# Optimization experiments

Hardware: AMD Instinct MI355X
Metric: run time of the kernel (lower is better)

Reference implementation:

```python
import jax, jax.numpy as jnp
import numpy as np

N = 200000          # nodes
G = 8192            # graphs (data.num_graphs)
NUM_RADIAL = 32
M_OUT = 85          # embedding_depth // 3 -> 85x1o


def setup_inputs() -> dict:
    key = jax.random.key(0)
    ks = jax.random.split(key, 24)
    f32 = jnp.float32
    def rn(k, shape, scale=1.0):
        return jax.random.normal(k, shape, dtype=f32) * scale
    inp = {}
    inp['pos'] = rn(ks[0], (N, 3))
    inp['z'] = jax.random.randint(ks[1], (N,), 0, 100)
    inp['batch'] = jnp.sort(jax.random.randint(ks[2], (N,), 0, G))
    inp['node_table'] = rn(ks[3], (100, 32))
    # MLP weights (fan-in scaled), biases zero
    inp['W_rbf0'] = rn(ks[4], (32, 64), 32 ** -0.5)
    inp['b_rbf0'] = jnp.zeros((64,), f32)
    inp['W_rbf1'] = rn(ks[5], (64, 64), 64 ** -0.5)
    inp['b_rbf1'] = jnp.zeros((64,), f32)
    inp['W_m0'] = rn(ks[6], (96, 64), 96 ** -0.5)
    inp['b_m0'] = jnp.zeros((64,), f32)
    inp['W_m1'] = rn(ks[7], (64, 64), 64 ** -0.5)
    inp['b_m1'] = jnp.zeros((64,), f32)
    inp['W_m2'] = rn(ks[8], (64, 64), 64 ** -0.5)
    inp['b_m2'] = jnp.zeros((64,), f32)
    # e3nn-style weights: N(0,1), path normalization applied in the math
    inp['w_tp0'] = rn(ks[9], (64, 64))   # 0e x 0e -> 0e
    inp['w_tp1'] = rn(ks[10], (64, 64))  # 0e x 1o -> 1o
    inp['w_tp2'] = rn(ks[11], (64, 32))  # 0e x 2e -> 2e
    inp['L0'] = rn(ks[12], (64, 64))     # o3.Linear 0e block
    inp['L1o'] = rn(ks[13], (64, 64))    # o3.Linear 1o block
    inp['L2e'] = rn(ks[14], (32, 32))    # o3.Linear 2e block
    inp['L_out'] = rn(ks[15], (64, 85))  # tl2: 64x1o -> 85x1o
    return inp


def _sph_harm(pos):
    # e3nn real spherical harmonics, normalize=False, normalization='component'
    x, y, z = pos[:, 0], pos[:, 1], pos[:, 2]
    sh0 = jnp.ones_like(x)                              # [N]     l=0
    sh1 = jnp.sqrt(3.0) * pos                           # [N,3]   l=1
    s15 = jnp.sqrt(15.0)
    s5 = jnp.sqrt(5.0)
    sh2 = jnp.stack([
        s15 * x * z,
        s15 * x * y,
        s5 * (y * y - 0.5 * (x * x + z * z)),
        s15 * y * z,
        0.5 * s15 * (z * z - x * x),
    ], axis=-1)                                          # [N,5]   l=2
    return sh0, sh1, sh2


def _forward(pos, z, batch, node_table, W_rbf0, b_rbf0, W_rbf1, b_rbf1,
             W_m0, b_m0, W_m1, b_m1, W_m2, b_m2,
             w_tp0, w_tp1, w_tp2, L0, L1o, L2e, L_out):
    sh0, sh1, sh2 = _sph_harm(pos)  # centroid is zeros

    # Gaussian RBF on |pos|, start=0 stop=1
    dist = jnp.linalg.norm(pos, axis=1)                  # [N]
    offsets = jnp.linspace(0.0, 1.0, NUM_RADIAL)
    coeff = -0.5 / (offsets[1] - offsets[0]) ** 2
    rbf = jnp.exp(coeff * (dist[:, None] - offsets) ** 2)  # [N,32]

    # rbf_emb MLP (1 hidden layer)
    r = jax.nn.gelu(rbf @ W_rbf0 + b_rbf0)
    r = r @ W_rbf1 + b_rbf1                               # [N,64]

    # radial_message MLP (2 hidden layers) on [r_emb, node_emb]
    h = jnp.concatenate([r, node_table[z]], axis=-1)      # [N,96]
    h = jax.nn.gelu(h @ W_m0 + b_m0)
    h = jax.nn.gelu(h @ W_m1 + b_m1)
    msg = h @ W_m2 + b_m2                                 # [N,64]  64x0e

    # FullyConnectedTensorProduct(64x0e, 1x0e+1x1o+1x2e -> irreps_mid)
    # scalar (x) l  -> l ; path norm 1/sqrt(fan_in), fan_in = 64*1
    inv = 1.0 / jnp.sqrt(64.0)
    c0 = (msg @ w_tp0) * sh0[:, None] * inv               # [N,64]    0e
    c1 = (msg @ w_tp1)[:, :, None] * sh1[:, None, :] * inv  # [N,64,3] 1o
    c2 = (msg @ w_tp2)[:, :, None] * sh2[:, None, :] * inv  # [N,32,5] 2e
    # 64x1e and 32x2o output blocks have no allowed paths -> identically zero

    # act1: gelu on scalar (0e) irreps only
    c0 = jax.nn.gelu(c0)

    # scatter mean + scatter sum over graphs
    cnt = jnp.maximum(jax.ops.segment_sum(jnp.ones_like(dist), batch, num_segments=G), 1.0)
    def agg(v, cshape):
        s = jax.ops.segment_sum(v, batch, num_segments=G)
        return s / cnt.reshape(cshape) + s
    g0 = agg(c0, (G, 1))        # [G,64]
    g1 = agg(c1, (G, 1, 1))     # [G,64,3]
    g2 = agg(c2, (G, 1, 1))     # [G,32,5]

    # tl1 (o3.Linear, per-irrep multiplicity mixing, 1/sqrt(mult_in) norm)
    g0 = g0 @ L0 * (64 ** -0.5)
    g1 = jnp.einsum('gum,uv->gvm', g1, L1o) * (64 ** -0.5)
    g2 = jnp.einsum('gum,uv->gvm', g2, L2e) * (32 ** -0.5)

    # act2: gelu on 0e only (g0 subsequently dropped by tl2's 1o-only output)
    g0 = jax.nn.gelu(g0)

    # tl2: irreps_mid -> 85x1o; only the 1o block contributes
    enc = jnp.einsum('gum,uv->gvm', g1, L_out) * (64 ** -0.5)  # [G,85,3]
    return enc.reshape(G, M_OUT * 3)


def reference(pos, z, batch, node_table, W_rbf0, b_rbf0, W_rbf1, b_rbf1,
              W_m0, b_m0, W_m1, b_m1, W_m2, b_m2,
              w_tp0, w_tp1, w_tp2, L0, L1o, L2e, L_out):
    return _forward(pos, z, batch, node_table, W_rbf0, b_rbf0, W_rbf1, b_rbf1,
                    W_m0, b_m0, W_m1, b_m1, W_m2, b_m2,
                    w_tp0, w_tp1, w_tp2, L0, L1o, L2e, L_out)
```

## Files before the change

kernel.cpp:

```cpp
#include <hip/hip_runtime.h>


typedef __attribute__((ext_vector_type(8))) short bf16x8;
typedef __attribute__((ext_vector_type(4))) float f32x4;
typedef unsigned short ushort_t;

#define SB 104

__device__ __forceinline__ unsigned rnebits(float x) {
    unsigned u = __float_as_uint(x);
    return u + 0x7fffu + ((u >> 16) & 1u);
}
__device__ __forceinline__ ushort_t f2bf(float x) { return (ushort_t)(rnebits(x) >> 16); }
__device__ __forceinline__ float bf2f(ushort_t h) { return __uint_as_float(((unsigned)h) << 16); }
__device__ __forceinline__ unsigned pack2bf(float lo, float hi) {
    return (rnebits(hi) & 0xffff0000u) | (rnebits(lo) >> 16);
}

__device__ __forceinline__ float gelu(float x) {
    float x2 = x * x;
    float y  = x * fmaf(0.10294324f, x2, 2.3022082f);
    float e  = __builtin_amdgcn_exp2f(y);
    float r  = __builtin_amdgcn_rcpf(e + 1.0f);
    return fmaf(-x, r, x);
}

__global__ __launch_bounds__(256)
void prep_kernel(const float* __restrict__ W_rbf0, const float* __restrict__ W_rbf1,
                 const float* __restrict__ W_m0, const float* __restrict__ W_m1,
                 const float* __restrict__ W_m2, const float* __restrict__ b_m2,
                 const float* __restrict__ w_tp1,
                 const float* __restrict__ L1o, const float* __restrict__ L_out,
                 const int* __restrict__ batch,
                 ushort_t* __restrict__ wb, float* __restrict__ bc,
                 float* __restrict__ Lcomb, int* __restrict__ seg, int N, int G)
{
    if (blockIdx.x >= 102) {
        int i = (blockIdx.x - 102) * 256 + threadIdx.x;
        if (i >= N) return;
        int bi = batch[i];
        int bprev = (i == 0) ? -1 : batch[i - 1];
        for (int g = bprev + 1; g <= bi; ++g) seg[g] = i;
        if (i == N - 1) for (int g = bi + 1; g <= G; ++g) seg[g] = N;
        return;
    }
    int idx = blockIdx.x * 256 + threadIdx.x;
    float w;
    ushort_t *dh, *dl;
    if (idx < 2048) {
        int f = idx >> 5, k = idx & 31;
        w = W_rbf0[k * 64 + f]; dh = wb + idx; dl = wb + 2048 + idx;
    } else if (idx < 6144) {
        int j = idx - 2048, f = j >> 6, k = j & 63;
        w = W_rbf1[k * 64 + f]; dh = wb + 4096 + j; dl = wb + 8192 + j;
    } else if (idx < 12288) {
        int j = idx - 6144, f = j / 96, k = j - 96 * f;
        w = W_m0[k * 64 + f]; dh = wb + 12288 + j; dl = wb + 18432 + j;
    } else if (idx < 16384) {
        int j = idx - 12288, f = j >> 6, k = j & 63;
        w = W_m1[k * 64 + f]; dh = wb + 24576 + j; dl = wb + 28672 + j;
    } else if (idx < 20480) {
        int j = idx - 16384, f = j >> 6, k = j & 63;
        float s = 0.f;
        for (int jj = 0; jj < 64; ++jj) s = fmaf(W_m2[k * 64 + jj], w_tp1[jj * 64 + f], s);
        w = s; dh = wb + 32768 + j; dl = wb + 36864 + j;
    } else if (idx < 20544) {
        int b = idx - 20480;
        float s = 0.f;
        for (int k = 0; k < 64; ++k) s = fmaf(b_m2[k], w_tp1[k * 64 + b], s);
        bc[b] = s;
        return;
    } else if (idx < 25984) {
        int j = idx - 20544, u = j / 85, v = j - 85 * u;
        float s = 0.f;
        for (int k = 0; k < 64; ++k) s = fmaf(L1o[u * 64 + k], L_out[k * 85 + v], s);
        Lcomb[j] = 0.015625f * s;
        return;
    } else return;
    ushort_t h = f2bf(w);
    *dh = h;
    *dl = f2bf(w - bf2f(h));
}

template<int KT, int ACT>
__device__ __forceinline__ void layer64(
    const ushort_t* __restrict__ Wh, const ushort_t* __restrict__ Wl,
    const float* __restrict__ bias, ushort_t* buf,
    ushort_t* __restrict__ Tout, int nodebase, int N, int lrow, int lcol)
{
    constexpr int K = KT * 32;
    __syncthreads();
    bf16x8 bb[4][KT];
    #pragma unroll
    for (int n = 0; n < 4; ++n)
        #pragma unroll
        for (int kt = 0; kt < KT; ++kt)
            bb[n][kt] = *(const bf16x8*)&buf[(n * 16 + lcol) * SB + kt * 32 + lrow * 8];
    __syncthreads();
    #pragma unroll
    for (int m = 0; m < 4; ++m) {
        const int f0 = m * 16 + lrow * 4;
        float4 bv = *(const float4*)(bias + f0);
        f32x4 acc[4];
        #pragma unroll
        for (int n = 0; n < 4; ++n) { acc[n][0] = bv.x; acc[n][1] = bv.y; acc[n][2] = bv.z; acc[n][3] = bv.w; }
        #pragma unroll
        for (int kt = 0; kt < KT; ++kt) {
            bf16x8 ah = *(const bf16x8*)(Wh + (m * 16 + lcol) * K + kt * 32 + lrow * 8);
            bf16x8 al = *(const bf16x8*)(Wl + (m * 16 + lcol) * K + kt * 32 + lrow * 8);
            #pragma unroll
            for (int n = 0; n < 4; ++n) {
                acc[n] = __builtin_amdgcn_mfma_f32_16x16x32_bf16(ah, bb[n][kt], acc[n], 0, 0, 0);
                acc[n] = __builtin_amdgcn_mfma_f32_16x16x32_bf16(al, bb[n][kt], acc[n], 0, 0, 0);
            }
        }
        #pragma unroll
        for (int n = 0; n < 4; ++n) {
            f32x4 v = acc[n];
            if (ACT == 1) {
                #pragma unroll
                for (int r = 0; r < 4; ++r) v[r] = gelu(v[r]);
            }
            uint2 pk;
            pk.x = pack2bf(v[0], v[1]);
            pk.y = pack2bf(v[2], v[3]);
            if (ACT == 2) {
                const int node = nodebase + n * 16 + lcol;
                if (node < N) *(uint2*)(Tout + (size_t)node * 64 + f0) = pk;
            } else {
                *(uint2*)&buf[(n * 16 + lcol) * SB + f0] = pk;
            }
        }
    }
}

__global__ __launch_bounds__(64, 3)
void node_mfma_kernel(const float* __restrict__ pos, const int* __restrict__ z,
                      const float* __restrict__ node_table,
                      const ushort_t* __restrict__ wb,
                      const float* __restrict__ b_rbf0, const float* __restrict__ b_rbf1,
                      const float* __restrict__ b_m0, const float* __restrict__ b_m1,
                      const float* __restrict__ bc,
                      ushort_t* __restrict__ Tout, int N)
{
    __shared__ ushort_t buf[64 * SB];
    const int lane = threadIdx.x;
    const int nodebase = blockIdx.x * 64;
    int gn = nodebase + lane;
    if (gn >= N) gn = N - 1;

    const float px = pos[3 * gn], py = pos[3 * gn + 1], pz = pos[3 * gn + 2];
    const float dist = sqrtf(px * px + py * py + pz * pz);
    {
        unsigned rb[16];
        #pragma unroll
        for (int j = 0; j < 16; ++j) {
            float d0 = dist - (float)(2 * j)     * (1.0f / 31.0f);
            float d1 = dist - (float)(2 * j + 1) * (1.0f / 31.0f);
            rb[j] = pack2bf(__builtin_amdgcn_exp2f(-693.2149671554846f * d0 * d0),
                            __builtin_amdgcn_exp2f(-693.2149671554846f * d1 * d1));
        }
        uint4* dst = (uint4*)&buf[lane * SB];
        dst[0] = make_uint4(rb[0], rb[1], rb[2], rb[3]);
        dst[1] = make_uint4(rb[4], rb[5], rb[6], rb[7]);
        dst[2] = make_uint4(rb[8], rb[9], rb[10], rb[11]);
        dst[3] = make_uint4(rb[12], rb[13], rb[14], rb[15]);
    }
    {
        const float* tb = node_table + (size_t)z[gn] * 32;
        unsigned tl[16];
        #pragma unroll
        for (int j = 0; j < 8; ++j) {
            float4 tv = *(const float4*)(tb + 4 * j);
            tl[2 * j]     = pack2bf(tv.x, tv.y);
            tl[2 * j + 1] = pack2bf(tv.z, tv.w);
        }
        uint4* dst = (uint4*)&buf[lane * SB + 64];
        dst[0] = make_uint4(tl[0], tl[1], tl[2], tl[3]);
        dst[1] = make_uint4(tl[4], tl[5], tl[6], tl[7]);
        dst[2] = make_uint4(tl[8], tl[9], tl[10], tl[11]);
        dst[3] = make_uint4(tl[12], tl[13], tl[14], tl[15]);
    }

    const int lrow = lane >> 4, lcol = lane & 15;
    layer64<1, 1>(wb + 0,     wb + 2048,  b_rbf0, buf, (ushort_t*)nullptr, 0, 0, lrow, lcol);
    layer64<2, 0>(wb + 4096,  wb + 8192,  b_rbf1, buf, (ushort_t*)nullptr, 0, 0, lrow, lcol);
    layer64<3, 1>(wb + 12288, wb + 18432, b_m0,   buf, (ushort_t*)nullptr, 0, 0, lrow, lcol);
    layer64<2, 1>(wb + 24576, wb + 28672, b_m1,   buf, (ushort_t*)nullptr, 0, 0, lrow, lcol);
    layer64<2, 2>(wb + 32768, wb + 36864, bc,     buf, Tout, nodebase, N, lrow, lcol);
}

__global__ __launch_bounds__(256)
void graph_kernel(const ushort_t* __restrict__ Tin, const float* __restrict__ pos,
                  const int* __restrict__ seg, const float* __restrict__ Lcomb,
                  float* __restrict__ out, int G) {
    __shared__ float g1s[4][64][3];
    const int lane = threadIdx.x & 63;
    const int wid = threadIdx.x >> 6;
    const int g = blockIdx.x * 4 + wid;
    const bool active = g < G;

    if (active) {
        const int s = seg[g], e = seg[g + 1];
        float a0 = 0.f, a1 = 0.f, a2 = 0.f;
        for (int nn = s; nn < e; ++nn) {
            float t = bf2f(Tin[(size_t)nn * 64 + lane]);
            float qx = pos[3 * nn + 0], qy = pos[3 * nn + 1], qz = pos[3 * nn + 2];
            a0 = fmaf(t, qx, a0);
            a1 = fmaf(t, qy, a1);
            a2 = fmaf(t, qz, a2);
        }
        float cnt = (float)((e - s) > 0 ? (e - s) : 1);
        float sc = 1.7320508075688772f * 0.125f * (1.0f + 1.0f / cnt);
        g1s[wid][lane][0] = a0 * sc;
        g1s[wid][lane][1] = a1 * sc;
        g1s[wid][lane][2] = a2 * sc;
    }
    __syncthreads();
    if (!active) return;

    float o0 = 0.f, o1 = 0.f, o2 = 0.f, p0 = 0.f, p1 = 0.f, p2 = 0.f;
    const int v2 = 64 + lane;
    for (int u = 0; u < 64; ++u) {
        float b0 = g1s[wid][u][0], b1 = g1s[wid][u][1], b2 = g1s[wid][u][2];
        float l0 = Lcomb[u * 85 + lane];
        o0 = fmaf(b0, l0, o0); o1 = fmaf(b1, l0, o1); o2 = fmaf(b2, l0, o2);
        if (lane < 21) {
            float l1 = Lcomb[u * 85 + v2];
            p0 = fmaf(b0, l1, p0); p1 = fmaf(b1, l1, p1); p2 = fmaf(b2, l1, p2);
        }
    }
    float* og = out + (size_t)g * 255;
    og[3 * lane + 0] = o0; og[3 * lane + 1] = o1; og[3 * lane + 2] = o2;
    if (lane < 21) {
        og[3 * v2 + 0] = p0; og[3 * v2 + 1] = p1; og[3 * v2 + 2] = p2;
    }
}

extern "C" void kernel_launch(void* const* d_in, const int* in_sizes, int n_in,
                              void* d_out, int out_size, void* d_ws, size_t ws_size,
                              hipStream_t stream) {
    const float* pos        = (const float*)d_in[0];
    const int*   z          = (const int*)d_in[1];
    const int*   batch      = (const int*)d_in[2];
    const float* node_table = (const float*)d_in[3];
    const float* W_rbf0     = (const float*)d_in[4];
    const float* b_rbf0     = (const float*)d_in[5];
    const float* W_rbf1     = (const float*)d_in[6];
    const float* b_rbf1     = (const float*)d_in[7];
    const float* W_m0       = (const float*)d_in[8];
    const float* b_m0       = (const float*)d_in[9];
    const float* W_m1       = (const float*)d_in[10];
    const float* b_m1       = (const float*)d_in[11];
    const float* W_m2       = (const float*)d_in[12];
    const float* b_m2       = (const float*)d_in[13];
    const float* w_tp1      = (const float*)d_in[15];
    const float* L1o        = (const float*)d_in[18];
    const float* L_out      = (const float*)d_in[20];
    float* out = (float*)d_out;

    const int N = in_sizes[0] / 3;
    const int G = out_size / 255;

    char* ws = (char*)d_ws;
    float*    bc    = (float*)(ws + 0);
    float*    Lcomb = (float*)(ws + 256);
    int*      seg   = (int*)(ws + 22528);
    ushort_t* wb    = (ushort_t*)(ws + 55424);
    ushort_t* T     = (ushort_t*)(ws + 137472);

    const int segBlocks = (N + 255) / 256;
    prep_kernel<<<102 + segBlocks, 256, 0, stream>>>(
        W_rbf0, W_rbf1, W_m0, W_m1, W_m2, b_m2, w_tp1, L1o, L_out,
        batch, wb, bc, Lcomb, seg, N, G);

    node_mfma_kernel<<<(N + 63) / 64, 64, 0, stream>>>(
        pos, z, node_table, wb, b_rbf0, b_rbf1, b_m0, b_m1, bc, T, N);

    graph_kernel<<<(G + 3) / 4, 256, 0, stream>>>(T, pos, seg, Lcomb, out, G);
}
```

Baseline: 83.52 us.

## Ping-pong LDS buffers, stream K-tiles, fetch table rows directly in MLP kernel

The per-node MLP kernel now alternates between two LDS buffers and replaces __syncthreads with a waitcnt fence, since each block is a single wavefront. The layer loop is restructured to stream B operands per K-tile into a 4x4 accumulator set, instead of loading every K-tile up front. The node-embedding table is converted to bf16 once in the prep kernel and gathered directly as MFMA operands for the third layer, rather than being staged through LDS. The final output goes out through LDS as coalesced 16-byte stores without a per-row bounds check. The cost is more accumulator registers, with launch bounds dropped from 3 to 2 waves, and the unguarded tail store assumes the workspace extends past N.

```diff
diff --git a/kernel.cpp b/kernel.cpp
--- a/kernel.cpp
+++ b/kernel.cpp
@@ -5,7 +5,7 @@
 typedef __attribute__((ext_vector_type(4))) float f32x4;
 typedef unsigned short ushort_t;
 
-#define SB 104
+#define SBW 72
 
 __device__ __forceinline__ unsigned rnebits(float x) {
     unsigned u = __float_as_uint(x);
@@ -15,6 +15,10 @@
 __device__ __forceinline__ float bf2f(ushort_t h) { return __uint_as_float(((unsigned)h) << 16); }
 __device__ __forceinline__ unsigned pack2bf(float lo, float hi) {
     return (rnebits(hi) & 0xffff0000u) | (rnebits(lo) >> 16);
+}
+__device__ __forceinline__ void lds_fence() {
+    asm volatile("s_waitcnt lgkmcnt(0)" ::: "memory");
+    __builtin_amdgcn_sched_barrier(0);
 }
 
 __device__ __forceinline__ float gelu(float x) {
@@ -31,12 +35,12 @@
                  const float* __restrict__ W_m2, const float* __restrict__ b_m2,
                  const float* __restrict__ w_tp1,
                  const float* __restrict__ L1o, const float* __restrict__ L_out,
-                 const int* __restrict__ batch,
+                 const float* __restrict__ node_table, const int* __restrict__ batch,
                  ushort_t* __restrict__ wb, float* __restrict__ bc,
                  float* __restrict__ Lcomb, int* __restrict__ seg, int N, int G)
 {
-    if (blockIdx.x >= 102) {
-        int i = (blockIdx.x - 102) * 256 + threadIdx.x;
+    if (blockIdx.x >= 115) {
+        int i = (blockIdx.x - 115) * 256 + threadIdx.x;
         if (i >= N) return;
         int bi = batch[i];
         int bprev = (i == 0) ? -1 : batch[i - 1];
@@ -76,47 +80,78 @@
         for (int k = 0; k < 64; ++k) s = fmaf(L1o[u * 64 + k], L_out[k * 85 + v], s);
         Lcomb[j] = 0.015625f * s;
         return;
+    } else if (idx < 29184) {
+        int j = idx - 25984;
+        wb[40960 + j] = f2bf(node_table[j]);
+        return;
     } else return;
     ushort_t h = f2bf(w);
     *dh = h;
     *dl = f2bf(w - bf2f(h));
 }
 
-template<int KT, int ACT>
-__device__ __forceinline__ void layer64(
+template<int KT, int ACT, bool TABLE>
+__device__ __forceinline__ void layerX(
     const ushort_t* __restrict__ Wh, const ushort_t* __restrict__ Wl,
-    const float* __restrict__ bias, ushort_t* buf,
-    ushort_t* __restrict__ Tout, int nodebase, int N, int lrow, int lcol)
+    const float* __restrict__ bias,
+    const ushort_t* src, ushort_t* dst,
+    const ushort_t* __restrict__ tab_bf, const int* __restrict__ zp,
+    int nodebase, int N, int lrow, int lcol)
 {
-    constexpr int K = KT * 32;
-    __syncthreads();
-    bf16x8 bb[4][KT];
+    constexpr int K = TABLE ? (KT * 32 + 32) : (KT * 32);
+    f32x4 acc[4][4];
     #pragma unroll
-    for (int n = 0; n < 4; ++n)
-        #pragma unroll
-        for (int kt = 0; kt < KT; ++kt)
-            bb[n][kt] = *(const bf16x8*)&buf[(n * 16 + lcol) * SB + kt * 32 + lrow * 8];
-    __syncthreads();
+    for (int m = 0; m < 4; ++m) {
+        float4 bv = *(const float4*)(bias + m * 16 + lrow * 4);
+        #pragma unroll
+        for (int n = 0; n < 4; ++n) {
+            acc[m][n][0] = bv.x; acc[m][n][1] = bv.y; acc[m][n][2] = bv.z; acc[m][n][3] = bv.w;
+        }
+    }
+    #pragma unroll
+    for (int kt = 0; kt < KT; ++kt) {
+        const int kof = kt * 32 + lrow * 8;
+        bf16x8 bb[4];
+        #pragma unroll
+        for (int n = 0; n < 4; ++n)
+            bb[n] = *(const bf16x8*)&src[(n * 16 + lcol) * SBW + kof];
+        #pragma unroll
+        for (int m = 0; m < 4; ++m) {
+            bf16x8 ah = *(const bf16x8*)(Wh + (m * 16 + lcol) * K + kof);
+            bf16x8 al = *(const bf16x8*)(Wl + (m * 16 + lcol) * K + kof);
+            #pragma unroll
+            for (int n = 0; n < 4; ++n) {
+                acc[m][n] = __builtin_amdgcn_mfma_f32_16x16x32_bf16(ah, bb[n], acc[m][n], 0, 0, 0);
+                acc[m][n] = __builtin_amdgcn_mfma_f32_16x16x32_bf16(al, bb[n], acc[m][n], 0, 0, 0);
+            }
+        }
+    }
+    if (TABLE) {
+        const int kof = KT * 32 + lrow * 8;
+        bf16x8 bb[4];
+        #pragma unroll
+        for (int n = 0; n < 4; ++n) {
+            int node = nodebase + n * 16 + lcol;
+            if (node > N - 1) node = N - 1;
+            bb[n] = *(const bf16x8*)(tab_bf + zp[node] * 32 + lrow * 8);
+        }
+        #pragma unroll
+        for (int m = 0; m < 4; ++m) {
+            bf16x8 ah = *(const bf16x8*)(Wh + (m * 16 + lcol) * K + kof);
+            bf16x8 al = *(const bf16x8*)(Wl + (m * 16 + lcol) * K + kof);
+            #pragma unroll
+            for (int n = 0; n < 4; ++n) {
+                acc[m][n] = __builtin_amdgcn_mfma_f32_16x16x32_bf16(ah, bb[n], acc[m][n], 0, 0, 0);
+                acc[m][n] = __builtin_amdgcn_mfma_f32_16x16x32_bf16(al, bb[n], acc[m][n], 0, 0, 0);
+            }
+        }
+    }
     #pragma unroll
     for (int m = 0; m < 4; ++m) {
         const int f0 = m * 16 + lrow * 4;
-        float4 bv = *(const float4*)(bias + f0);
-        f32x4 acc[4];
-        #pragma unroll
-        for (int n = 0; n < 4; ++n) { acc[n][0] = bv.x; acc[n][1] = bv.y; acc[n][2] = bv.z; acc[n][3] = bv.w; }
-        #pragma unroll
-        for (int kt = 0; kt < KT; ++kt) {
-            bf16x8 ah = *(const bf16x8*)(Wh + (m * 16 + lcol) * K + kt * 32 + lrow * 8);
-            bf16x8 al = *(const bf16x8*)(Wl + (m * 16 + lcol) * K + kt * 32 + lrow * 8);
-            #pragma unroll
-            for (int n = 0; n < 4; ++n) {
-                acc[n] = __builtin_amdgcn_mfma_f32_16x16x32_bf16(ah, bb[n][kt], acc[n], 0, 0, 0);
-                acc[n] = __builtin_amdgcn_mfma_f32_16x16x32_bf16(al, bb[n][kt], acc[n], 0, 0, 0);
-            }
-        }
         #pragma unroll
         for (int n = 0; n < 4; ++n) {
-            f32x4 v = acc[n];
+            f32x4 v = acc[m][n];
             if (ACT == 1) {
                 #pragma unroll
                 for (int r = 0; r < 4; ++r) v[r] = gelu(v[r]);
@@ -124,34 +159,30 @@
             uint2 pk;
             pk.x = pack2bf(v[0], v[1]);
             pk.y = pack2bf(v[2], v[3]);
-            if (ACT == 2) {
-                const int node = nodebase + n * 16 + lcol;
-                if (node < N) *(uint2*)(Tout + (size_t)node * 64 + f0) = pk;
-            } else {
-                *(uint2*)&buf[(n * 16 + lcol) * SB + f0] = pk;
-            }
-        }
-    }
-}
-
-__global__ __launch_bounds__(64, 3)
+            *(uint2*)&dst[(n * 16 + lcol) * SBW + f0] = pk;
+        }
+    }
+}
+
+__global__ __launch_bounds__(64, 2)
 void node_mfma_kernel(const float* __restrict__ pos, const int* __restrict__ z,
-                      const float* __restrict__ node_table,
                       const ushort_t* __restrict__ wb,
                       const float* __restrict__ b_rbf0, const float* __restrict__ b_rbf1,
                       const float* __restrict__ b_m0, const float* __restrict__ b_m1,
                       const float* __restrict__ bc,
                       ushort_t* __restrict__ Tout, int N)
 {
-    __shared__ ushort_t buf[64 * SB];
+    __shared__ ushort_t bufA[64 * SBW];
+    __shared__ ushort_t bufB[64 * SBW];
     const int lane = threadIdx.x;
     const int nodebase = blockIdx.x * 64;
     int gn = nodebase + lane;
     if (gn >= N) gn = N - 1;
-
-    const float px = pos[3 * gn], py = pos[3 * gn + 1], pz = pos[3 * gn + 2];
-    const float dist = sqrtf(px * px + py * py + pz * pz);
+    const ushort_t* tab_bf = wb + 40960;
+
     {
+        const float px = pos[3 * gn], py = pos[3 * gn + 1], pz = pos[3 * gn + 2];
+        const float dist = sqrtf(px * px + py * py + pz * pz);
         unsigned rb[16];
         #pragma unroll
         for (int j = 0; j < 16; ++j) {
@@ -160,34 +191,34 @@
             rb[j] = pack2bf(__builtin_amdgcn_exp2f(-693.2149671554846f * d0 * d0),
                             __builtin_amdgcn_exp2f(-693.2149671554846f * d1 * d1));
         }
-        uint4* dst = (uint4*)&buf[lane * SB];
+        uint4* dst = (uint4*)&bufA[lane * SBW];
         dst[0] = make_uint4(rb[0], rb[1], rb[2], rb[3]);
         dst[1] = make_uint4(rb[4], rb[5], rb[6], rb[7]);
         dst[2] = make_uint4(rb[8], rb[9], rb[10], rb[11]);
         dst[3] = make_uint4(rb[12], rb[13], rb[14], rb[15]);
     }
+    lds_fence();
+
+    const int lrow = lane >> 4, lcol = lane & 15;
+    layerX<1, 1, false>(wb + 0, wb + 2048, b_rbf0, bufA, bufB, tab_bf, z, nodebase, N, lrow, lcol);
+    lds_fence();
+    layerX<2, 0, false>(wb + 4096, wb + 8192, b_rbf1, bufB, bufA, tab_bf, z, nodebase, N, lrow, lcol);
+    lds_fence();
+    layerX<2, 1, true>(wb + 12288, wb + 18432, b_m0, bufA, bufB, tab_bf, z, nodebase, N, lrow, lcol);
+    lds_fence();
+    layerX<2, 1, false>(wb + 24576, wb + 28672, b_m1, bufB, bufA, tab_bf, z, nodebase, N, lrow, lcol);
+    lds_fence();
+    layerX<2, 0, false>(wb + 32768, wb + 36864, bc, bufA, bufB, tab_bf, z, nodebase, N, lrow, lcol);
+    lds_fence();
+
     {
-        const float* tb = node_table + (size_t)z[gn] * 32;
-        unsigned tl[16];
-        #pragma unroll
-        for (int j = 0; j < 8; ++j) {
-            float4 tv = *(const float4*)(tb + 4 * j);
-            tl[2 * j]     = pack2bf(tv.x, tv.y);
-            tl[2 * j + 1] = pack2bf(tv.z, tv.w);
-        }
-        uint4* dst = (uint4*)&buf[lane * SB + 64];
-        dst[0] = make_uint4(tl[0], tl[1], tl[2], tl[3]);
-        dst[1] = make_uint4(tl[4], tl[5], tl[6], tl[7]);
-        dst[2] = make_uint4(tl[8], tl[9], tl[10], tl[11]);
-        dst[3] = make_uint4(tl[12], tl[13], tl[14], tl[15]);
-    }
-
-    const int lrow = lane >> 4, lcol = lane & 15;
-    layer64<1, 1>(wb + 0,     wb + 2048,  b_rbf0, buf, (ushort_t*)nullptr, 0, 0, lrow, lcol);
-    layer64<2, 0>(wb + 4096,  wb + 8192,  b_rbf1, buf, (ushort_t*)nullptr, 0, 0, lrow, lcol);
-    layer64<3, 1>(wb + 12288, wb + 18432, b_m0,   buf, (ushort_t*)nullptr, 0, 0, lrow, lcol);
-    layer64<2, 1>(wb + 24576, wb + 28672, b_m1,   buf, (ushort_t*)nullptr, 0, 0, lrow, lcol);
-    layer64<2, 2>(wb + 32768, wb + 36864, bc,     buf, Tout, nodebase, N, lrow, lcol);
+        ushort_t* tb = Tout + (size_t)nodebase * 64;
+        #pragma unroll
+        for (int i = 0; i < 8; ++i) {
+            bf16x8 v = *(const bf16x8*)&bufB[(i * 8 + (lane >> 3)) * SBW + (lane & 7) * 8];
+            *(bf16x8*)(tb + i * 512 + lane * 8) = v;
+        }
+    }
 }
 
 __global__ __launch_bounds__(256)
@@ -266,16 +297,16 @@
     float*    bc    = (float*)(ws + 0);
     float*    Lcomb = (float*)(ws + 256);
     int*      seg   = (int*)(ws + 22528);
-    ushort_t* wb    = (ushort_t*)(ws + 55424);
-    ushort_t* T     = (ushort_t*)(ws + 137472);
+    ushort_t* wb    = (ushort_t*)(ws + 55552);
+    ushort_t* T     = (ushort_t*)(ws + 144128);
 
     const int segBlocks = (N + 255) / 256;
-    prep_kernel<<<102 + segBlocks, 256, 0, stream>>>(
+    prep_kernel<<<115 + segBlocks, 256, 0, stream>>>(
         W_rbf0, W_rbf1, W_m0, W_m1, W_m2, b_m2, w_tp1, L1o, L_out,
-        batch, wb, bc, Lcomb, seg, N, G);
+        node_table, batch, wb, bc, Lcomb, seg, N, G);
 
     node_mfma_kernel<<<(N + 63) / 64, 64, 0, stream>>>(
-        pos, z, node_table, wb, b_rbf0, b_rbf1, b_m0, b_m1, bc, T, N);
+        pos, z, wb, b_rbf0, b_rbf1, b_m0, b_m1, bc, T, N);
 
     graph_kernel<<<(G + 3) / 4, 256, 0, stream>>>(T, pos, seg, Lcomb, out, G);
 }
```

Result: faster. 81.63 us (-2.3%).
